# Kernel optimization log

Measured on AMD Instinct MI355X. Metric: run time of the kernel, lower is better.

## Reference

```python
import jax, jax.numpy as jnp
import numpy as np

ALPHA = 0.2  # leaky-relu negative slope
NEG_INF = -9e15


def setup_inputs() -> dict:
    key = jax.random.key(0)
    ks = jax.random.split(key, 10)
    bz, N, Fin, Fout = 16, 1024, 1024, 1024
    h = jax.random.normal(ks[0], (bz, N, Fin), dtype=jnp.float32)
    h_xReact = jax.random.normal(ks[1], (bz, N, Fout), dtype=jnp.float32)
    h_oReact = jax.random.normal(ks[2], (bz, N, Fout), dtype=jnp.float32)
    utt_xReact_mask = (jax.random.uniform(ks[3], (bz, N, N)) > 0.5).astype(jnp.float32)
    utt_oReact_mask = (jax.random.uniform(ks[4], (bz, N, N)) > 0.5).astype(jnp.float32)
    W = jax.random.normal(ks[5], (Fin, Fout), dtype=jnp.float32) * 0.02
    a_SS = jax.random.normal(ks[6], (2 * Fout, 1), dtype=jnp.float32) * 0.05
    a_DS = jax.random.normal(ks[7], (2 * Fout, 1), dtype=jnp.float32) * 0.05
    csk_W = jax.random.normal(ks[8], (Fout, Fout), dtype=jnp.float32) * 0.02
    csk_b = jnp.zeros((Fout,), dtype=jnp.float32)
    return {"h": h, "h_xReact": h_xReact, "h_oReact": h_oReact,
            "utt_xReact_mask": utt_xReact_mask, "utt_oReact_mask": utt_oReact_mask,
            "W": W, "a_SS": a_SS, "a_DS": a_DS, "csk_W": csk_W, "csk_b": csk_b}


def _scores(Wh, h_react, a, mask):
    # e[b,i,j] = leaky_relu(Wh[b,i].a1 + (Wh[b,j]+h_react[b,j]).a2) * mask[b,i,j]
    F = Wh.shape[-1]
    a1, a2 = a[:F, 0], a[F:, 0]
    s_src = Wh @ a1                      # [bz, N]
    s_dst = (Wh + h_react) @ a2          # [bz, N]
    e = jax.nn.leaky_relu(s_src[:, :, None] + s_dst[:, None, :], negative_slope=ALPHA)
    return e * mask


def reference(h, h_xReact, h_oReact, utt_xReact_mask, utt_oReact_mask,
              W, a_SS, a_DS, csk_W, csk_b):
    Wh = h @ W                                       # [bz, N, F]
    hx = h_xReact @ csk_W.T + csk_b                  # csk_linear
    ho = h_oReact @ csk_W.T + csk_b
    e_SS = _scores(Wh, hx, a_SS, utt_xReact_mask)    # [bz, N, N]
    e_DS = _scores(Wh, ho, a_DS, utt_oReact_mask)
    e = e_SS + e_DS
    # faithful to source bug: adj uses xReact mask twice
    adj = utt_xReact_mask + utt_xReact_mask
    att = jax.nn.softmax(jnp.where(adj > 0, e, NEG_INF), axis=-1)
    # dropout: eval mode (deterministic reference) -> identity
    h_prime = att @ Wh                               # [bz, N, F]
    return jax.nn.elu(h_prime)                       # concat=True
```

## Files before the change

kernel.cpp:

```cpp
#include <hip/hip_runtime.h>
#include <hip/hip_bf16.h>
#include <math.h>

#define BZ 16
#define NN 1024
#define FF 1024
#define ALPHA 0.2f
#define NEG_INF (-9e15f)

typedef __bf16 bf16x8 __attribute__((ext_vector_type(8)));
typedef __bf16 bf16x4 __attribute__((ext_vector_type(4)));
typedef float  f32x4  __attribute__((ext_vector_type(4)));
typedef int    i32x4  __attribute__((ext_vector_type(4)));

#define GLOBAL_AS __attribute__((address_space(1)))
#define LDS_AS    __attribute__((address_space(3)))

__device__ inline void load_lds16(const void* g, void* l) {
    __builtin_amdgcn_global_load_lds((const GLOBAL_AS void*)g, (LDS_AS void*)l, 16, 0, 0);
}

__device__ inline void nt_store64(void* p, const void* v) {
    __builtin_nontemporal_store(*(const unsigned long long*)v, (unsigned long long*)p);
}
__device__ inline void nt_store128(void* p, const void* v) {
    __builtin_nontemporal_store(*(const i32x4*)v, (i32x4*)p);
}

__device__ inline float waveAllSum(float v) {
    for (int o = 32; o; o >>= 1) v += __shfl_xor(v, o);
    return v;
}
__device__ inline float waveAllMax(float v) {
    for (int o = 32; o; o >>= 1) v = fmaxf(v, __shfl_xor(v, o));
    return v;
}
__device__ inline float waveReduceSum(float v) {
    for (int o = 32; o; o >>= 1) v += __shfl_down(v, o);
    return v;
}
__device__ inline float dot4(f32x4 a, f32x4 b) {
    return a.x * b.x + a.y * b.y + a.z * b.z + a.w * b.w;
}

template<int EPI>
__global__ __launch_bounds__(512, 2) void gemm256(
    const __bf16* __restrict__ A, const __bf16* __restrict__ Bt,
    float* __restrict__ Cf, __bf16* __restrict__ Ct, size_t sB)
{
    __shared__ char lds[131072];

    const int bid = blockIdx.x;
    const int l   = (bid & 7) * 32 + (bid >> 3);
    const int tileM = (l >> 2) * 256;
    const int tileN = (l & 3) * 256;

    const int tid = threadIdx.x, lane = tid & 63, wid = tid >> 6;
    const int wr = wid >> 2, wc = wid & 3;

    const int batch = tileM >> 10;
    const char* Ab  = (const char*)(A + (size_t)tileM * FF);
    const char* Bbp = (const char*)(Bt + (size_t)batch * sB + (size_t)tileN * FF);

    const int o1 = wid * 1024 + lane * 16;
    const int o2 = o1 + 8192;
    const int r1 = o1 >> 7, r2 = o2 >> 7;
    const size_t raoff1 = (size_t)r1 * 2048 + ((o1 & 127) ^ ((r1 & 7) << 4));
    const size_t raoff2 = (size_t)r2 * 2048 + ((o2 & 127) ^ ((r2 & 7) << 4));

#define STAGE(gb, ldsoff, half, kt) do {                                        \
    const char* g_ = (gb) + (size_t)(half) * (128 * 2048) + (size_t)(kt) * 128; \
    load_lds16(g_ + raoff1, lds + (ldsoff) + (half) * 16384 + wid * 1024);      \
    load_lds16(g_ + raoff2, lds + (ldsoff) + (half) * 16384 + 8192 + wid * 1024);\
} while (0)

    const int fr = lane & 15, kq = lane >> 4;
    const int fswz = (fr & 7) << 4;
    const int ck[2] = { (kq * 16) ^ fswz, (64 + kq * 16) ^ fswz };
    const int abase = (wr * 128 + fr) * 128;
    const int bbase = 32768 + (wc * 64 + fr) * 128;

#define RD(off) (*(const bf16x8*)(lds + (off)))
#define RDA(P, m, kh) RD((P) * 65536 + abase + (m) * 2048 + ck[kh])
#define RDB(P, n, kh) RD((P) * 65536 + bbase + (n) * 2048 + ck[kh])
#define MF16(amr, bvr, m0) do {                                              \
    _Pragma("unroll") for (int n = 0; n < 4; ++n)                            \
    _Pragma("unroll") for (int m = 0; m < 4; ++m)                            \
        acc[m0 + m][n] = __builtin_amdgcn_mfma_f32_16x16x32_bf16(            \
            amr[m], bvr[n], acc[m0 + m][n], 0, 0, 0); } while (0)
#define BAR   __builtin_amdgcn_s_barrier()
#define LGKM0 do { asm volatile("s_waitcnt lgkmcnt(0)" ::: "memory");        \
                   __builtin_amdgcn_sched_barrier(0); } while (0)
#define VM4   asm volatile("s_waitcnt vmcnt(4)" ::: "memory")
#define VM0   asm volatile("s_waitcnt vmcnt(0)" ::: "memory")
#define PRIO1 __builtin_amdgcn_s_setprio(1)
#define PRIO0 __builtin_amdgcn_s_setprio(0)

    f32x4 acc[8][4];
    #pragma unroll
    for (int m = 0; m < 8; ++m)
        #pragma unroll
        for (int n = 0; n < 4; ++n) acc[m][n] = (f32x4){0.f, 0.f, 0.f, 0.f};

    bf16x8 a0[4], a47k0[4], a47k1[4], b0[4], b1[4];

    STAGE(Ab,      0, 0, 0);  STAGE(Ab,      0, 1, 0);
    STAGE(Bbp, 32768, 0, 0);  STAGE(Bbp, 32768, 1, 0);
    STAGE(Bbp, 65536 + 32768, 0, 1);
    STAGE(Ab,  65536,         0, 1);
    VM4; BAR;

    const int NT = FF / 64;
    for (int it = 0; it < NT / 2; ++it) {
        const int t   = 2 * it;
        const int kt1 = t + 1;
        const int kt2 = (t + 2 < NT) ? t + 2 : NT - 1;
        const int kt3 = (t + 3 < NT) ? t + 3 : NT - 1;

        #pragma unroll
        for (int m = 0; m < 4; ++m) a0[m] = RDA(0, m, 0);
        #pragma unroll
        for (int n = 0; n < 4; ++n) b0[n] = RDB(0, n, 0);
        STAGE(Ab, 65536, 1, kt1);
        BAR; LGKM0; PRIO1; MF16(a0, b0, 0); PRIO0; BAR;

        #pragma unroll
        for (int m = 0; m < 4; ++m) a0[m] = RDA(0, m, 1);
        #pragma unroll
        for (int n = 0; n < 4; ++n) b1[n] = RDB(0, n, 1);
        STAGE(Bbp, 65536 + 32768, 1, kt1);
        BAR; LGKM0; PRIO1; MF16(a0, b1, 0); PRIO0; BAR;

        #pragma unroll
        for (int m = 0; m < 4; ++m) { a47k0[m] = RDA(0, 4 + m, 0); a47k1[m] = RDA(0, 4 + m, 1); }
        STAGE(Bbp, 32768, 0, kt2);
        BAR; LGKM0; PRIO1; MF16(a47k0, b0, 4); PRIO0; BAR;

        STAGE(Ab, 0, 0, kt2);
        BAR; PRIO1; MF16(a47k1, b1, 4); PRIO0; VM4; BAR;

        #pragma unroll
        for (int m = 0; m < 4; ++m) a0[m] = RDA(1, m, 0);
        #pragma unroll
        for (int n = 0; n < 4; ++n) b0[n] = RDB(1, n, 0);
        STAGE(Ab, 0, 1, kt2);
        BAR; LGKM0; PRIO1; MF16(a0, b0, 0); PRIO0; BAR;

        #pragma unroll
        for (int m = 0; m < 4; ++m) a0[m] = RDA(1, m, 1);
        #pragma unroll
        for (int n = 0; n < 4; ++n) b1[n] = RDB(1, n, 1);
        STAGE(Bbp, 32768, 1, kt2);
        BAR; LGKM0; PRIO1; MF16(a0, b1, 0); PRIO0; BAR;

        #pragma unroll
        for (int m = 0; m < 4; ++m) { a47k0[m] = RDA(1, 4 + m, 0); a47k1[m] = RDA(1, 4 + m, 1); }
        STAGE(Bbp, 65536 + 32768, 0, kt3);
        BAR; LGKM0; PRIO1; MF16(a47k0, b0, 4); PRIO0; BAR;

        STAGE(Ab, 65536, 0, kt3);
        BAR; PRIO1; MF16(a47k1, b1, 4); PRIO0; VM4; BAR;
    }

    if (EPI == 1) {
        #pragma unroll
        for (int fm = 0; fm < 8; ++fm) {
            const int row0 = tileM + wr * 128 + fm * 16 + kq * 4;
            #pragma unroll
            for (int fn = 0; fn < 4; ++fn) {
                const int col = tileN + wc * 64 + fn * 16 + fr;
                #pragma unroll
                for (int r = 0; r < 4; ++r) {
                    float v = acc[fm][fn][r];
                    v = (v > 0.f) ? v : expm1f(v);
                    __builtin_nontemporal_store(v, &Cf[(size_t)(row0 + r) * FF + col]);
                }
            }
        }
    } else {
        VM0; BAR;
        char* wlds = lds + wid * 16384;
        #pragma unroll
        for (int fm = 0; fm < 8; ++fm)
            #pragma unroll
            for (int fn = 0; fn < 4; ++fn) {
                const int ccol = fn * 16 + fr;
                const int crow = fm * 16 + kq * 4;
                int addr = (ccol * 256 + crow * 2) ^ ((ccol & 7) << 4);
                bf16x4 v = { (__bf16)acc[fm][fn][0], (__bf16)acc[fm][fn][1],
                             (__bf16)acc[fm][fn][2], (__bf16)acc[fm][fn][3] };
                *(bf16x4*)(wlds + addr) = v;
            }
        const int jb = (tileM & 1023) + wr * 128;
        __bf16* Wt = Ct + (size_t)batch * (1024 * 1024);
        #pragma unroll
        for (int pass = 0; pass < 16; ++pass) {
            const int fl  = pass * 4 + (lane >> 4);
            const int jby = (lane & 15) * 16;
            int addr = (fl * 256 + jby) ^ ((fl & 7) << 4);
            bf16x8 v = *(const bf16x8*)(wlds + addr);
            const int fg = tileN + wc * 64 + fl;
            nt_store128((char*)(Wt + (size_t)fg * 1024 + jb) + jby, &v);
        }
    }
#undef STAGE
#undef RD
#undef RDA
#undef RDB
#undef MF16
}

__global__ __launch_bounds__(256) void scores_h(
    const float* __restrict__ h, const float* __restrict__ wa,
    __bf16* __restrict__ h_bf,
    float* __restrict__ sSrcSS, float* __restrict__ pD1,
    float* __restrict__ sSrcDS, float* __restrict__ pD3)
{
    const int wid = threadIdx.x >> 6, lane = threadIdx.x & 63;
    const int row = blockIdx.x * 4 + wid;
    const f32x4* hr  = (const f32x4*)(h + (size_t)row * FF);
    const f32x4* w0p = (const f32x4*)wa;
    const f32x4* w1p = (const f32x4*)(wa + FF);
    const f32x4* w2p = (const f32x4*)(wa + 2 * FF);
    const f32x4* w3p = (const f32x4*)(wa + 3 * FF);

    f32x4 hv[4], w0[4], w1[4], w2[4], w3[4];
    #pragma unroll
    for (int q = 0; q < 4; ++q) hv[q] = hr[q * 64 + lane];
    #pragma unroll
    for (int q = 0; q < 4; ++q) {
        const int i = q * 64 + lane;
        w0[q] = w0p[i]; w1[q] = w1p[i]; w2[q] = w2p[i]; w3[q] = w3p[i];
    }

    bf16x4* hbp = (bf16x4*)(h_bf + (size_t)row * FF);
    #pragma unroll
    for (int q = 0; q < 4; ++q) {
        f32x4 v = hv[q];
        bf16x4 hb = { (__bf16)v.x, (__bf16)v.y, (__bf16)v.z, (__bf16)v.w };
        nt_store64(&hbp[q * 64 + lane], &hb);
    }

    float d0 = 0.f, d1 = 0.f, d2 = 0.f, d3 = 0.f;
    #pragma unroll
    for (int q = 0; q < 4; ++q) {
        d0 += dot4(hv[q], w0[q]);
        d1 += dot4(hv[q], w1[q]);
        d2 += dot4(hv[q], w2[q]);
        d3 += dot4(hv[q], w3[q]);
    }
    d0 = waveAllSum(d0); d1 = waveAllSum(d1);
    d2 = waveAllSum(d2); d3 = waveAllSum(d3);
    if (lane == 0) {
        sSrcSS[row] = d0;
        pD1[row]    = d1;
        sSrcDS[row] = d2;
        pD3[row]    = d3;
    }
}

__global__ __launch_bounds__(256) void scores_react(
    const float* __restrict__ hx, const float* __restrict__ ho,
    const float* __restrict__ vSS, const float* __restrict__ vDS,
    float* __restrict__ pD4, float* __restrict__ pD5)
{
    const int wid = threadIdx.x >> 6, lane = threadIdx.x & 63;
    const int row = blockIdx.x * 4 + wid;
    const f32x4* xr  = (const f32x4*)(hx + (size_t)row * FF);
    const f32x4* orr = (const f32x4*)(ho + (size_t)row * FF);
    const f32x4* vsp = (const f32x4*)vSS;
    const f32x4* vdp = (const f32x4*)vDS;

    f32x4 xv[4], ov[4], vs[4], vd[4];
    #pragma unroll
    for (int q = 0; q < 4; ++q) {
        const int i = q * 64 + lane;
        xv[q] = xr[i]; ov[q] = orr[i];
    }
    #pragma unroll
    for (int q = 0; q < 4; ++q) {
        const int i = q * 64 + lane;
        vs[q] = vsp[i]; vd[q] = vdp[i];
    }

    float d4 = 0.f, d5 = 0.f;
    #pragma unroll
    for (int q = 0; q < 4; ++q) {
        d4 += dot4(xv[q], vs[q]);
        d5 += dot4(ov[q], vd[q]);
    }
    d4 = waveAllSum(d4); d5 = waveAllSum(d5);
    if (lane == 0) {
        pD4[row] = d4;
        pD5[row] = d5;
    }
}

__global__ __launch_bounds__(256) void transpose_cvt(
    const float* __restrict__ in, __bf16* __restrict__ out, int R, int C)
{
    const float* ib = in;
    __bf16* ob = out;
    const int r0 = blockIdx.y * 64;
    const int c0 = blockIdx.x * 64;
    __shared__ __bf16 t[64][66];
    #pragma unroll
    for (int it = 0; it < 16; ++it) {
        int idx = threadIdx.x + it * 256;
        int r = idx >> 6, c = idx & 63;
        t[r][c] = (__bf16)ib[(size_t)(r0 + r) * C + c0 + c];
    }
    __syncthreads();
    #pragma unroll
    for (int it = 0; it < 4; ++it) {
        int idx = threadIdx.x + it * 256;
        int rr = idx >> 4;
        int cc = (idx & 15) * 4;
        bf16x4 v = { t[cc][rr], t[cc + 1][rr], t[cc + 2][rr], t[cc + 3][rr] };
        nt_store64(&ob[(size_t)(c0 + rr) * R + r0 + cc], &v);
    }
}

__global__ __launch_bounds__(256) void prep_wa(
    const float* __restrict__ W, const float* __restrict__ aSS,
    const float* __restrict__ aDS, float* __restrict__ wa)
{
    const int i = blockIdx.x;
    const int t = threadIdx.x;
    float4 w  = ((const float4*)(W + (size_t)i * FF))[t];
    float4 s1 = ((const float4*)aSS)[t];
    float4 s2 = ((const float4*)(aSS + FF))[t];
    float4 d1 = ((const float4*)aDS)[t];
    float4 d2 = ((const float4*)(aDS + FF))[t];
    float v0 = w.x * s1.x + w.y * s1.y + w.z * s1.z + w.w * s1.w;
    float v1 = w.x * s2.x + w.y * s2.y + w.z * s2.z + w.w * s2.w;
    float v2 = w.x * d1.x + w.y * d1.y + w.z * d1.z + w.w * d1.w;
    float v3 = w.x * d2.x + w.y * d2.y + w.z * d2.z + w.w * d2.w;
    v0 = waveReduceSum(v0); v1 = waveReduceSum(v1);
    v2 = waveReduceSum(v2); v3 = waveReduceSum(v3);
    __shared__ float red[4][4];
    int wid = t >> 6;
    if ((t & 63) == 0) { red[wid][0] = v0; red[wid][1] = v1; red[wid][2] = v2; red[wid][3] = v3; }
    __syncthreads();
    if (t < 4) {
        float s = red[0][t] + red[1][t] + red[2][t] + red[3][t];
        wa[(size_t)t * FF + i] = s;
    }
}

__global__ __launch_bounds__(256) void prep_v(
    const float* __restrict__ cskW, const float* __restrict__ aSS,
    const float* __restrict__ aDS, float* __restrict__ vSS, float* __restrict__ vDS)
{
    const int g0 = blockIdx.x * 64;
    const int gl = threadIdx.x & 63;
    const int fs = threadIdx.x >> 6;
    const int g = g0 + gl;
    float aS = 0.f, aD = 0.f;
    for (int f = fs * 256; f < fs * 256 + 256; ++f) {
        float w = cskW[(size_t)f * FF + g];
        aS += w * aSS[FF + f];
        aD += w * aDS[FF + f];
    }
    __shared__ float rS[4][64], rD[4][64];
    rS[fs][gl] = aS; rD[fs][gl] = aD;
    __syncthreads();
    if (fs == 0) {
        vSS[g] = rS[0][gl] + rS[1][gl] + rS[2][gl] + rS[3][gl];
        vDS[g] = rD[0][gl] + rD[1][gl] + rD[2][gl] + rD[3][gl];
    }
}

__global__ __launch_bounds__(256) void prep_c(
    const float* __restrict__ cskb, const float* __restrict__ aSS,
    const float* __restrict__ aDS, float* __restrict__ cv)
{
    int t = threadIdx.x;
    float cS = 0.f, cD = 0.f;
    for (int f = t; f < FF; f += 256) {
        float bb = cskb[f];
        cS += bb * aSS[FF + f];
        cD += bb * aDS[FF + f];
    }
    cS = waveReduceSum(cS);
    cD = waveReduceSum(cD);
    __shared__ float rA[4], rB[4];
    int wid = t >> 6;
    if ((t & 63) == 0) { rA[wid] = cS; rB[wid] = cD; }
    __syncthreads();
    if (t == 0) {
        cv[0] = rA[0] + rA[1] + rA[2] + rA[3];
        cv[1] = rB[0] + rB[1] + rB[2] + rB[3];
    }
}

__global__ __launch_bounds__(256) void softmax_att(
    const float* __restrict__ mx, const float* __restrict__ mo,
    const float* __restrict__ sSrcSS, const float* __restrict__ sSrcDS,
    const float* __restrict__ pD1, const float* __restrict__ pD3,
    const float* __restrict__ pD4, const float* __restrict__ pD5,
    const float* __restrict__ cv, __bf16* __restrict__ att)
{
    const int wid = threadIdx.x >> 6, lane = threadIdx.x & 63;
    const int row = blockIdx.x * 4 + wid;
    const int base = row & ~(NN - 1);
    const float srcS = sSrcSS[row];
    const float srcD = sSrcDS[row];
    const float cv0 = cv[0], cv1 = cv[1];
    const f32x4* mxr = (const f32x4*)(mx + (size_t)row * NN);
    const f32x4* mor = (const f32x4*)(mo + (size_t)row * NN);
    const f32x4* p1p = (const f32x4*)(pD1 + base);
    const f32x4* p3p = (const f32x4*)(pD3 + base);
    const f32x4* p4p = (const f32x4*)(pD4 + base);
    const f32x4* p5p = (const f32x4*)(pD5 + base);

    float ev[16];
    float m = -INFINITY;
    #pragma unroll
    for (int q = 0; q < 4; ++q) {
        const int idx = q * 64 + lane;
        f32x4 a = mxr[idx], o = mor[idx];
        f32x4 p1 = p1p[idx], p3 = p3p[idx], p4 = p4p[idx], p5 = p5p[idx];
        #pragma unroll
        for (int l = 0; l < 4; ++l) {
            float eS = srcS + p1[l] + p4[l] + cv0;
            float lS = (eS >= 0.f) ? eS : ALPHA * eS;
            float eD = srcD + p3[l] + p5[l] + cv1;
            float lD = (eD >= 0.f) ? eD : ALPHA * eD;
            float val = (a[l] > 0.f) ? (lS * a[l] + lD * o[l]) : NEG_INF;
            ev[q * 4 + l] = val;
            m = fmaxf(m, val);
        }
    }
    m = waveAllMax(m);

    float s = 0.f;
    #pragma unroll
    for (int i = 0; i < 16; ++i) {
        float p = expf(ev[i] - m);
        ev[i] = p;
        s += p;
    }
    s = waveAllSum(s);
    const float inv = 1.f / s;

    bf16x4* ar = (bf16x4*)(att + (size_t)row * NN);
    #pragma unroll
    for (int q = 0; q < 4; ++q) {
        bf16x4 v = { (__bf16)(ev[q * 4 + 0] * inv), (__bf16)(ev[q * 4 + 1] * inv),
                     (__bf16)(ev[q * 4 + 2] * inv), (__bf16)(ev[q * 4 + 3] * inv) };
        nt_store64(&ar[q * 64 + lane], &v);
    }
}

extern "C" void kernel_launch(void* const* d_in, const int* in_sizes, int n_in,
                              void* d_out, int out_size, void* d_ws, size_t ws_size,
                              hipStream_t stream)
{
    const float* h    = (const float*)d_in[0];
    const float* hx   = (const float*)d_in[1];
    const float* ho   = (const float*)d_in[2];
    const float* mx   = (const float*)d_in[3];
    const float* mo   = (const float*)d_in[4];
    const float* W    = (const float*)d_in[5];
    const float* aSS  = (const float*)d_in[6];
    const float* aDS  = (const float*)d_in[7];
    const float* cskW = (const float*)d_in[8];
    const float* cskb = (const float*)d_in[9];
    float* out = (float*)d_out;

    char* ws = (char*)d_ws;
    const size_t MB = 1024 * 1024;
    __bf16* h_bf   = (__bf16*)ws;
    __bf16* WhT_bf = (__bf16*)(ws + 32 * MB);
    __bf16* att_bf = (__bf16*)(ws + 64 * MB);
    __bf16* WbfT   = (__bf16*)(ws + 96 * MB);
    float* wa     = (float*)(ws + 98 * MB);
    float* vSS    = wa + 4 * FF;
    float* vDS    = vSS + FF;
    float* cv     = vDS + FF;
    float* sSrcSS = cv + 64;
    float* sSrcDS = sSrcSS + BZ * NN;
    float* pD1    = sSrcDS + BZ * NN;
    float* pD3    = pD1 + BZ * NN;
    float* pD4    = pD3 + BZ * NN;
    float* pD5    = pD4 + BZ * NN;

    prep_wa<<<FF, 256, 0, stream>>>(W, aSS, aDS, wa);
    prep_v<<<16, 256, 0, stream>>>(cskW, aSS, aDS, vSS, vDS);
    prep_c<<<1, 256, 0, stream>>>(cskb, aSS, aDS, cv);
    transpose_cvt<<<dim3(16, 16, 1), 256, 0, stream>>>(W, WbfT, FF, FF);
    scores_h<<<BZ * NN / 4, 256, 0, stream>>>(h, wa, h_bf, sSrcSS, pD1, sSrcDS, pD3);
    scores_react<<<BZ * NN / 4, 256, 0, stream>>>(hx, ho, vSS, vDS, pD4, pD5);
    gemm256<2><<<256, 512, 0, stream>>>(h_bf, WbfT, nullptr, WhT_bf, 0);
    softmax_att<<<BZ * NN / 4, 256, 0, stream>>>(mx, mo, sSrcSS, sSrcDS,
                                                 pD1, pD3, pD4, pD5, cv, att_bf);
    gemm256<1><<<256, 512, 0, stream>>>(att_bf, WhT_bf, out, nullptr,
                                        (size_t)NN * FF);
}
```

Baseline: 200.1 us.

## Replace hand-scheduled 2-stage GEMM pipeline with 4-buffer K=32 ring

Rewrites the gemm256 main loop. The hand-interleaved double-buffered schedule with K=64 tiles and half-tile staging is replaced by a simple 4-slot ring of K=32 tiles that prefetches three stages ahead, with one barrier pair per step. The XOR swizzle on LDS rows is dropped, so LDS reads may now hit bank conflicts. Nontemporal stores in both epilogues become ordinary stores. The simpler loop has more barriers per unit of K and less overlap of LDS reads with MFMA.

```diff
diff --git a/kernel.cpp b/kernel.cpp
--- a/kernel.cpp
+++ b/kernel.cpp
@@ -23,9 +23,6 @@
 __device__ inline void nt_store64(void* p, const void* v) {
     __builtin_nontemporal_store(*(const unsigned long long*)v, (unsigned long long*)p);
 }
-__device__ inline void nt_store128(void* p, const void* v) {
-    __builtin_nontemporal_store(*(const i32x4*)v, (i32x4*)p);
-}
 
 __device__ inline float waveAllSum(float v) {
     for (int o = 32; o; o >>= 1) v += __shfl_xor(v, o);
@@ -62,36 +59,28 @@
     const char* Ab  = (const char*)(A + (size_t)tileM * FF);
     const char* Bbp = (const char*)(Bt + (size_t)batch * sB + (size_t)tileN * FF);
 
-    const int o1 = wid * 1024 + lane * 16;
-    const int o2 = o1 + 8192;
-    const int r1 = o1 >> 7, r2 = o2 >> 7;
-    const size_t raoff1 = (size_t)r1 * 2048 + ((o1 & 127) ^ ((r1 & 7) << 4));
-    const size_t raoff2 = (size_t)r2 * 2048 + ((o2 & 127) ^ ((r2 & 7) << 4));
-
-#define STAGE(gb, ldsoff, half, kt) do {                                        \
-    const char* g_ = (gb) + (size_t)(half) * (128 * 2048) + (size_t)(kt) * 128; \
-    load_lds16(g_ + raoff1, lds + (ldsoff) + (half) * 16384 + wid * 1024);      \
-    load_lds16(g_ + raoff2, lds + (ldsoff) + (half) * 16384 + 8192 + wid * 1024);\
+    const size_t srowoff = (size_t)(tid >> 2) * 2048 + (size_t)(tid & 3) * 16;
+
+#define STAGEA(buf, kt) do {                                                  \
+    const char* g_ = Ab + srowoff + (size_t)(kt) * 64;                        \
+    load_lds16(g_,              lds + (buf) * 16384 + wid * 1024);            \
+    load_lds16(g_ + 128 * 2048, lds + (buf) * 16384 + 8192 + wid * 1024);     \
 } while (0)
+#define STAGEB(buf, kt) do {                                                  \
+    const char* g_ = Bbp + srowoff + (size_t)(kt) * 64;                       \
+    load_lds16(g_,              lds + 65536 + (buf) * 16384 + wid * 1024);    \
+    load_lds16(g_ + 128 * 2048, lds + 65536 + (buf) * 16384 + 8192 + wid * 1024);\
+} while (0)
 
     const int fr = lane & 15, kq = lane >> 4;
-    const int fswz = (fr & 7) << 4;
-    const int ck[2] = { (kq * 16) ^ fswz, (64 + kq * 16) ^ fswz };
-    const int abase = (wr * 128 + fr) * 128;
-    const int bbase = 32768 + (wc * 64 + fr) * 128;
+    const int aoff = (wr * 128 + fr) * 64 + kq * 16;
+    const int boff = (wc * 64 + fr) * 64 + kq * 16;
 
 #define RD(off) (*(const bf16x8*)(lds + (off)))
-#define RDA(P, m, kh) RD((P) * 65536 + abase + (m) * 2048 + ck[kh])
-#define RDB(P, n, kh) RD((P) * 65536 + bbase + (n) * 2048 + ck[kh])
-#define MF16(amr, bvr, m0) do {                                              \
-    _Pragma("unroll") for (int n = 0; n < 4; ++n)                            \
-    _Pragma("unroll") for (int m = 0; m < 4; ++m)                            \
-        acc[m0 + m][n] = __builtin_amdgcn_mfma_f32_16x16x32_bf16(            \
-            amr[m], bvr[n], acc[m0 + m][n], 0, 0, 0); } while (0)
 #define BAR   __builtin_amdgcn_s_barrier()
 #define LGKM0 do { asm volatile("s_waitcnt lgkmcnt(0)" ::: "memory");        \
                    __builtin_amdgcn_sched_barrier(0); } while (0)
-#define VM4   asm volatile("s_waitcnt vmcnt(4)" ::: "memory")
+#define VM8   asm volatile("s_waitcnt vmcnt(8)" ::: "memory")
 #define VM0   asm volatile("s_waitcnt vmcnt(0)" ::: "memory")
 #define PRIO1 __builtin_amdgcn_s_setprio(1)
 #define PRIO0 __builtin_amdgcn_s_setprio(0)
@@ -102,64 +91,32 @@
         #pragma unroll
         for (int n = 0; n < 4; ++n) acc[m][n] = (f32x4){0.f, 0.f, 0.f, 0.f};
 
-    bf16x8 a0[4], a47k0[4], a47k1[4], b0[4], b1[4];
-
-    STAGE(Ab,      0, 0, 0);  STAGE(Ab,      0, 1, 0);
-    STAGE(Bbp, 32768, 0, 0);  STAGE(Bbp, 32768, 1, 0);
-    STAGE(Bbp, 65536 + 32768, 0, 1);
-    STAGE(Ab,  65536,         0, 1);
-    VM4; BAR;
-
-    const int NT = FF / 64;
-    for (int it = 0; it < NT / 2; ++it) {
-        const int t   = 2 * it;
-        const int kt1 = t + 1;
-        const int kt2 = (t + 2 < NT) ? t + 2 : NT - 1;
-        const int kt3 = (t + 3 < NT) ? t + 3 : NT - 1;
-
-        #pragma unroll
-        for (int m = 0; m < 4; ++m) a0[m] = RDA(0, m, 0);
-        #pragma unroll
-        for (int n = 0; n < 4; ++n) b0[n] = RDB(0, n, 0);
-        STAGE(Ab, 65536, 1, kt1);
-        BAR; LGKM0; PRIO1; MF16(a0, b0, 0); PRIO0; BAR;
-
-        #pragma unroll
-        for (int m = 0; m < 4; ++m) a0[m] = RDA(0, m, 1);
-        #pragma unroll
-        for (int n = 0; n < 4; ++n) b1[n] = RDB(0, n, 1);
-        STAGE(Bbp, 65536 + 32768, 1, kt1);
-        BAR; LGKM0; PRIO1; MF16(a0, b1, 0); PRIO0; BAR;
-
-        #pragma unroll
-        for (int m = 0; m < 4; ++m) { a47k0[m] = RDA(0, 4 + m, 0); a47k1[m] = RDA(0, 4 + m, 1); }
-        STAGE(Bbp, 32768, 0, kt2);
-        BAR; LGKM0; PRIO1; MF16(a47k0, b0, 4); PRIO0; BAR;
-
-        STAGE(Ab, 0, 0, kt2);
-        BAR; PRIO1; MF16(a47k1, b1, 4); PRIO0; VM4; BAR;
-
-        #pragma unroll
-        for (int m = 0; m < 4; ++m) a0[m] = RDA(1, m, 0);
-        #pragma unroll
-        for (int n = 0; n < 4; ++n) b0[n] = RDB(1, n, 0);
-        STAGE(Ab, 0, 1, kt2);
-        BAR; LGKM0; PRIO1; MF16(a0, b0, 0); PRIO0; BAR;
-
-        #pragma unroll
-        for (int m = 0; m < 4; ++m) a0[m] = RDA(1, m, 1);
-        #pragma unroll
-        for (int n = 0; n < 4; ++n) b1[n] = RDB(1, n, 1);
-        STAGE(Bbp, 32768, 1, kt2);
-        BAR; LGKM0; PRIO1; MF16(a0, b1, 0); PRIO0; BAR;
-
-        #pragma unroll
-        for (int m = 0; m < 4; ++m) { a47k0[m] = RDA(1, 4 + m, 0); a47k1[m] = RDA(1, 4 + m, 1); }
-        STAGE(Bbp, 65536 + 32768, 0, kt3);
-        BAR; LGKM0; PRIO1; MF16(a47k0, b0, 4); PRIO0; BAR;
-
-        STAGE(Ab, 65536, 0, kt3);
-        BAR; PRIO1; MF16(a47k1, b1, 4); PRIO0; VM4; BAR;
+    bf16x8 a[8], b[4];
+
+    STAGEA(0, 0); STAGEB(0, 0);
+    STAGEA(1, 1); STAGEB(1, 1);
+    STAGEA(2, 2); STAGEB(2, 2);
+    VM8; BAR;
+
+    const int NT = FF / 32;
+    #pragma unroll 4
+    for (int t = 0; t < NT; ++t) {
+        const int cur = t & 3;
+        const int kt = (t + 3 < NT) ? t + 3 : NT - 1;
+        const int nb = (t + 3) & 3;
+        STAGEA(nb, kt); STAGEB(nb, kt);
+        #pragma unroll
+        for (int m = 0; m < 8; ++m) a[m] = RD(cur * 16384 + aoff + m * 1024);
+        #pragma unroll
+        for (int n = 0; n < 4; ++n) b[n] = RD(65536 + cur * 16384 + boff + n * 1024);
+        BAR; LGKM0; PRIO1;
+        #pragma unroll
+        for (int n = 0; n < 4; ++n)
+            #pragma unroll
+            for (int m = 0; m < 8; ++m)
+                acc[m][n] = __builtin_amdgcn_mfma_f32_16x16x32_bf16(
+                    a[m], b[n], acc[m][n], 0, 0, 0);
+        PRIO0; VM8; BAR;
     }
 
     if (EPI == 1) {
@@ -173,7 +130,7 @@
                 for (int r = 0; r < 4; ++r) {
                     float v = acc[fm][fn][r];
                     v = (v > 0.f) ? v : expm1f(v);
-                    __builtin_nontemporal_store(v, &Cf[(size_t)(row0 + r) * FF + col]);
+                    Cf[(size_t)(row0 + r) * FF + col] = v;
                 }
             }
         }
@@ -200,14 +157,12 @@
             int addr = (fl * 256 + jby) ^ ((fl & 7) << 4);
             bf16x8 v = *(const bf16x8*)(wlds + addr);
             const int fg = tileN + wc * 64 + fl;
-            nt_store128((char*)(Wt + (size_t)fg * 1024 + jb) + jby, &v);
+            *(bf16x8*)((char*)(Wt + (size_t)fg * 1024 + jb) + jby) = v;
         }
     }
-#undef STAGE
+#undef STAGEA
+#undef STAGEB
 #undef RD
-#undef RDA
-#undef RDB
-#undef MF16
 }
 
 __global__ __launch_bounds__(256) void scores_h(
```

Result: slower. 210.9 us (+5.4%).
